# Kernel optimization log

Measured on AMD Instinct MI355X. Metric: run time of the kernel, lower is better.

Reference implementation:

```python
import jax, jax.numpy as jnp
import numpy as np

EPS = 1e-5

def _conv(x, w, b, pad):
    # x: [B,C,H,W], w: [O,I,kh,kw] -> [B,O,H',W']
    y = jax.lax.conv_general_dilated(x, w, (1, 1), pad,
                                     dimension_numbers=('NCHW', 'OIHW', 'NCHW'))
    return y + b[None, :, None, None]

def _bn(x, g, b, m, v):
    # inference-mode BatchNorm2d
    s = g / jnp.sqrt(v + EPS)
    return x * s[None, :, None, None] + (b - m * s)[None, :, None, None]

def setup_inputs():
    key = jax.random.key(0)
    ks = jax.random.split(key, 8)
    N, Cin, Cout, H, W, BS = 2, 64, 256, 512, 512, 32
    GH, GW = H // BS, W // BS
    nB = 256
    x = jax.random.normal(ks[0], (N, Cin, H, W), jnp.float32)
    rng = np.random.default_rng(0)
    flat = rng.choice(N * GH * GW, size=nB, replace=False)  # unique blocks
    idx = np.stack([flat // (GH * GW), (flat // GW) % GH, flat % GW], axis=1).astype(np.int32)
    indices = jnp.asarray(idx)             # [nB, 3] = (batch, block_row, block_col)
    mask = jnp.zeros((N, GH, GW), jnp.bool_).at[indices[:, 0], indices[:, 1], indices[:, 2]].set(True)
    def wgt(k, shape):
        return jax.random.normal(k, shape, jnp.float32) * 0.05
    z, o = jnp.zeros(Cout, jnp.float32), jnp.ones(Cout, jnp.float32)
    params = dict(
        w1=wgt(ks[1], (Cout, Cin, 1, 1)), b1=z, g1=o, be1=z, m1=z, v1=o,
        w2=wgt(ks[2], (Cout, Cout, 3, 3)), b2=z, g2=o, be2=z, m2=z, v2=o,
        w3=wgt(ks[3], (Cout, Cout, 1, 1)), b3=z, g3=o, be3=z, m3=z, v3=o,
        wd=wgt(ks[4], (Cout, Cin, 1, 1)), bd=z,
    )
    return {"x": x, "mask": mask, "indices": indices, **params,
            "block_size": 32, "block_stride": 32, "block_offset": 0}

def reference(x, mask, indices, w1, b1, g1, be1, m1, v1,
              w2, b2, g2, be2, m2, v2, w3, b3, g3, be3, m3, v3,
              wd, bd, block_size, block_stride, block_offset):
    BS = block_size
    N, Cin, H, W = x.shape
    b = indices[:, 0]
    rows = indices[:, 1, None] * block_stride + block_offset + jnp.arange(BS)  # [nB,BS]
    cols = indices[:, 2, None] * block_stride + block_offset + jnp.arange(BS)  # [nB,BS]
    ci = jnp.arange(Cin)
    # SparseGather: [nB, Cin, BS, BS]
    blocks = x[b[:, None, None, None], ci[None, :, None, None],
               rows[:, None, :, None], cols[:, None, None, :]]
    h = jax.nn.relu(_bn(_conv(blocks, w1, b1, 'VALID'), g1, be1, m1, v1))
    dense_y = jax.nn.relu(_bn(_conv(h, w2, b2, 'SAME'), g2, be2, m2, v2))
    # conv3/bn3 in the original are dead code (inplace-relu aliasing): output unused.
    ybase = _conv(x, wd, bd, 'VALID')  # downsample (in_channels != out_channels)
    Cout = ybase.shape[1]
    co = jnp.arange(Cout)
    # SparseScatter (add=False -> overwrite blocks; indices are unique)
    y = ybase.at[b[:, None, None, None], co[None, :, None, None],
                 rows[:, None, :, None], cols[:, None, None, :]].set(dense_y)
    return y
```

## Files before the change

kernel.cpp:

```cpp
#include <hip/hip_runtime.h>

#define HW 262144
#define EPSF 1e-5f

typedef __attribute__((ext_vector_type(8))) short bf16x8;
typedef __attribute__((ext_vector_type(4))) float f32x4;

__device__ __forceinline__ unsigned short f2bf(float f) {
    unsigned u = __builtin_bit_cast(unsigned, f);
    return (unsigned short)((u + 0x7FFFu + ((u >> 16) & 1u)) >> 16);
}

typedef __attribute__((address_space(3))) unsigned lds_u32_t;
typedef __attribute__((address_space(1))) const unsigned glb_u32_t;
__device__ __forceinline__ void dma16(const void* gsrc, void* ldst) {
    __builtin_amdgcn_global_load_lds((glb_u32_t*)gsrc, (lds_u32_t*)ldst, 16, 0, 0);
}

#define W2WS_OFF 0
#define W1WS_OFF 1212416
#define T1WS_OFF 1249280
#define S2WS_OFF 1250304
#define T2WS_OFF 1251328
#define WDWS_OFF 1252352
#define MSKWS_OFF 1289216

__global__ __launch_bounds__(512) void kmask(const int* __restrict__ indices,
                                             int nB, char* __restrict__ ws) {
    unsigned char* mb = (unsigned char*)(ws + MSKWS_OFF);
    const int t = threadIdx.x;
    if (t < 512) mb[t] = 0;
    __syncthreads();
    if (t < nB) {
        int bn = indices[t*3+0], gh = indices[t*3+1], gw = indices[t*3+2];
        if ((unsigned)bn < 2u && (unsigned)gh < 16u && (unsigned)gw < 16u)
            mb[bn*256 + gh*16 + gw] = 1;
    }
}

__global__ __launch_bounds__(256) void kprep(
    const float* __restrict__ w1, const float* __restrict__ b1,
    const float* __restrict__ g1, const float* __restrict__ be1,
    const float* __restrict__ m1, const float* __restrict__ v1,
    const float* __restrict__ w2, const float* __restrict__ b2,
    const float* __restrict__ g2, const float* __restrict__ be2,
    const float* __restrict__ m2, const float* __restrict__ v2,
    const float* __restrict__ wd,
    char* __restrict__ ws)
{
    unsigned short* w2ws = (unsigned short*)(ws + W2WS_OFF);
    unsigned short* w1ws = (unsigned short*)(ws + W1WS_OFF);
    unsigned short* wdws = (unsigned short*)(ws + WDWS_OFF);
    float* t1ws = (float*)(ws + T1WS_OFF);
    float* s2ws = (float*)(ws + S2WS_OFF);
    float* t2ws = (float*)(ws + T2WS_OFF);

    const int bid = blockIdx.x, t = threadIdx.x;
    if (bid < 2304) {
        int e  = bid*256 + t;
        int hc = e & 31;
        int r1 = e >> 5;
        int tap = r1 % 9;
        int r2 = r1 / 9;
        int co = r2 & 63;
        int q  = r2 >> 6;
        int cz = q & 3, ch = q >> 2;
        float v = w2[(size_t)(cz*64+co)*2304 + (size_t)(ch*32+hc)*9 + tap];
        w2ws[((ch*4+cz)*64+co)*296 + tap*32 + hc] = f2bf(v);
    } else if (bid < 2368) {
        int e = (bid-2304)*256 + t;
        int hc = e >> 6, ci = e & 63;
        float s1 = g1[hc] * rsqrtf(v1[hc] + EPSF);
        w1ws[hc*72 + ci] = f2bf(w1[hc*64+ci] * s1);
    } else if (bid < 2432) {
        int e = (bid-2368)*256 + t;
        int co = e >> 6, ci = e & 63;
        wdws[co*72 + ci] = f2bf(wd[co*64 + ci]);
    } else {
        if (t < 256) {
            float s1 = g1[t] * rsqrtf(v1[t] + EPSF);
            t1ws[t] = (b1[t]-m1[t])*s1 + be1[t];
            float s2 = g2[t] * rsqrtf(v2[t] + EPSF);
            s2ws[t] = s2;
            t2ws[t] = (b2[t]-m2[t])*s2 + be2[t];
        }
    }
}

__global__ __launch_bounds__(256, 2) void k1_mfma(
    const float* __restrict__ x,
    const float* __restrict__ bd, const char* __restrict__ ws,
    const int* __restrict__ bstride, const int* __restrict__ boff,
    float* __restrict__ y)
{
    extern __shared__ char smem[];
    unsigned short* xT  = (unsigned short*)smem;
    unsigned short* wdS = (unsigned short*)(smem + 36864);
    float*          bdS = (float*)(smem + 73728);

    const int t = threadIdx.x, lane = t & 63, w = t >> 6;
    const int m = lane & 15, g = lane >> 4;
    const int bid = blockIdx.x;
    const int n   = bid >> 10;
    const int row = (bid >> 1) & 511;
    const int c0  = (bid & 1) * 256;

    #pragma unroll
    for (int i = 0; i < 9; ++i)
        dma16((const char*)ws + WDWS_OFF + (t + i*256)*16,
              (char*)wdS + (t + i*256)*16);
    if (t < 64) dma16((const char*)bd + t*16, (char*)bdS + t*16);

    const size_t xbase = (size_t)n*64*HW + (size_t)row*512 + c0;
    #pragma unroll 4
    for (int jc = 0; jc < 16; ++jc) {
        int ci = w + 4*jc;
        float4 xv = *(const float4*)&x[xbase + (size_t)ci*HW + lane*4];
        xT[(lane*4+0)*72 + ci] = f2bf(xv.x);
        xT[(lane*4+1)*72 + ci] = f2bf(xv.y);
        xT[(lane*4+2)*72 + ci] = f2bf(xv.z);
        xT[(lane*4+3)*72 + ci] = f2bf(xv.w);
    }

    const int stride = bstride[0], off = boff[0];
    const bool safe = (stride == 32) && (off == 0);
    unsigned long long mv = 0;
    if (safe) {
        const unsigned char* mb = (const unsigned char*)(ws + MSKWS_OFF);
        mv = *(const unsigned long long*)&mb[n*256 + (row>>5)*16 + (bid&1)*8];
    }

    __syncthreads();

    bf16x8 bF[2][4];
    #pragma unroll
    for (int pxf = 0; pxf < 4; ++pxf)
        #pragma unroll
        for (int kk = 0; kk < 2; ++kk)
            bF[kk][pxf] = *(const bf16x8*)&xT[(w*64 + pxf*16 + m)*72 + kk*32 + g*8];

    const size_t ybase = (size_t)(n*256)*HW + (size_t)row*512 + c0;
    #pragma unroll 1
    for (int cof = 0; cof < 16; ++cof) {
        bf16x8 a0 = *(const bf16x8*)&wdS[(cof*16+m)*72 +      g*8];
        bf16x8 a1 = *(const bf16x8*)&wdS[(cof*16+m)*72 + 32 + g*8];
        f32x4 ac[4];
        #pragma unroll
        for (int pxf = 0; pxf < 4; ++pxf) {
            ac[pxf] = (f32x4){0.f,0.f,0.f,0.f};
            ac[pxf] = __builtin_amdgcn_mfma_f32_16x16x32_bf16(a0, bF[0][pxf], ac[pxf], 0, 0, 0);
            ac[pxf] = __builtin_amdgcn_mfma_f32_16x16x32_bf16(a1, bF[1][pxf], ac[pxf], 0, 0, 0);
        }
        #pragma unroll
        for (int pxf = 0; pxf < 4; ++pxf) {
            const int pxg = w*4 + pxf;
            const bool skip = safe && (((mv >> ((pxg>>1)*8)) & 0xffull) != 0ull);
            if (!skip) {
                #pragma unroll
                for (int j = 0; j < 4; ++j) {
                    const int co = cof*16 + g*4 + j;
                    y[ybase + (size_t)co*HW + pxg*16 + m] = ac[pxf][j] + bdS[co];
                }
            }
        }
    }
}

__global__ __launch_bounds__(512, 2) void k2_fused(
    const float* __restrict__ x, const int* __restrict__ indices,
    const char* __restrict__ ws,
    const int* __restrict__ bstride, const int* __restrict__ boff,
    float* __restrict__ y)
{
    extern __shared__ char smem[];
    unsigned short* xT  = (unsigned short*)smem;
    unsigned short* w1s = (unsigned short*)(smem + 50688);
    unsigned short* hS  = (unsigned short*)(smem + 55296);
    unsigned short* w2S = (unsigned short*)(smem + 77824);
    float* t1S = (float*)(smem + 115712);
    float* s2S = (float*)(smem + 116736);
    float* t2S = (float*)(smem + 117760);

    const unsigned short* w2ws = (const unsigned short*)(ws + W2WS_OFF);
    const unsigned short* w1ws = (const unsigned short*)(ws + W1WS_OFF);

    const int t    = threadIdx.x;
    const int lane = t & 63;
    const int w    = t >> 6;
    const int m    = lane & 15;
    const int g    = lane >> 4;

    const int bid = blockIdx.x;
    const int blk = bid >> 2, pz = bid & 3;
    const int bn = indices[blk*3+0], gr = indices[blk*3+1], gc = indices[blk*3+2];
    const int stride = bstride[0], off = boff[0];
    const int row0 = gr*stride + off, col0 = gc*stride + off;

    if (t < 192) {
        const float* src = (t < 64) ? (const float*)(ws + T1WS_OFF)
                         : (t < 128) ? (const float*)(ws + S2WS_OFF)
                                     : (const float*)(ws + T2WS_OFF);
        float* dst = (t < 64) ? t1S : (t < 128) ? s2S : t2S;
        dma16(src + (lane)*4, dst + (lane)*4);
    }

    {
        const int half = lane >> 5, cc = lane & 31;
        for (int pb = w*80; pb < w*80 + 80; pb += 2) {
            int pi = pb + half;
            int r = pi >> 6, ci = pi & 63;
            int br = pz*8 + r - 1;
            if ((unsigned)br < 32u) {
                float xv = x[(size_t)bn*64*HW + (size_t)ci*HW
                             + (size_t)(row0+br)*512 + (col0+cc)];
                xT[(r*34 + cc + 1)*72 + ci] = f2bf(xv);
            }
        }
    }

    f32x4 acc[4][2][4];
    #pragma unroll
    for (int a = 0; a < 4; ++a)
        #pragma unroll
        for (int b = 0; b < 2; ++b)
            #pragma unroll
            for (int c = 0; c < 4; ++c) acc[a][b][c] = (f32x4){0.f,0.f,0.f,0.f};

    #pragma unroll 1
    for (int ch = 0; ch < 8; ++ch) {
        __syncthreads();

        if (t < 288) dma16((const char*)w1ws + ch*4608 + t*16, (char*)w1s + t*16);
        {
            const char* ws2 = (const char*)w2ws + (size_t)(ch*4 + 0)*37888;
            #pragma unroll
            for (int i = 0; i < 4; ++i)
                dma16(ws2 + t*16 + i*8192, (char*)w2S + t*16 + i*8192);
            if (t < 320) dma16(ws2 + t*16 + 32768, (char*)w2S + t*16 + 32768);
        }
        __syncthreads();

        f32x4 a1[3][2];
        #pragma unroll
        for (int i = 0; i < 3; ++i) { a1[i][0] = (f32x4){0,0,0,0}; a1[i][1] = (f32x4){0,0,0,0}; }
        #pragma unroll
        for (int i = 0; i < 3; ++i) {
            const int tile = w*3 + i;
            if (tile < 22) {
                #pragma unroll
                for (int kk = 0; kk < 2; ++kk) {
                    bf16x8 bF = *(const bf16x8*)&xT[(tile*16 + m)*72 + kk*32 + g*8];
                    #pragma unroll
                    for (int hct = 0; hct < 2; ++hct) {
                        bf16x8 aF = *(const bf16x8*)&w1s[(hct*16 + m)*72 + kk*32 + g*8];
                        a1[i][hct] = __builtin_amdgcn_mfma_f32_16x16x32_bf16(
                                         aF, bF, a1[i][hct], 0, 0, 0);
                    }
                }
            }
        }
        #pragma unroll
        for (int i = 0; i < 3; ++i) {
            const int tile = w*3 + i;
            if (tile < 22) {
                int p = tile*16 + m;
                int r = p / 34;
                int c = p - r*34;
                int br = pz*8 + r - 1;
                bool valid = (c >= 1) && (c <= 32) && ((unsigned)br < 32u);
                #pragma unroll
                for (int hct = 0; hct < 2; ++hct) {
                    unsigned short hv[4];
                    #pragma unroll
                    for (int j = 0; j < 4; ++j) {
                        float tv = t1S[ch*32 + hct*16 + g*4 + j];
                        float hf = fmaxf(a1[i][hct][j] + tv, 0.f);
                        hv[j] = valid ? f2bf(hf) : (unsigned short)0;
                    }
                    unsigned lo = (unsigned)hv[0] | ((unsigned)hv[1] << 16);
                    unsigned hi = (unsigned)hv[2] | ((unsigned)hv[3] << 16);
                    *(uint2*)&hS[p*32 + hct*16 + g*4] = make_uint2(lo, hi);
                }
            }
        }
        __syncthreads();

        #pragma unroll
        for (int cz = 0; cz < 4; ++cz) {
            #pragma unroll
            for (int tap = 0; tap < 9; ++tap) {
                const int dy = tap/3, dx = tap%3;
                bf16x8 aF[4];
                #pragma unroll
                for (int cof = 0; cof < 4; ++cof)
                    aF[cof] = *(const bf16x8*)&w2S[(cof*16 + m)*296 + tap*32 + g*8];
                #pragma unroll
                for (int pxf = 0; pxf < 2; ++pxf) {
                    int p = (w + dy)*34 + pxf*16 + m + dx;
                    bf16x8 bF = *(const bf16x8*)&hS[p*32 + g*8];
                    if (cz == 0) {
                        #pragma unroll
                        for (int cof = 0; cof < 4; ++cof)
                            acc[0][pxf][cof] = __builtin_amdgcn_mfma_f32_16x16x32_bf16(
                                aF[cof], bF, acc[0][pxf][cof], 0, 0, 0);
                    } else if (cz == 1) {
                        #pragma unroll
                        for (int cof = 0; cof < 4; ++cof)
                            acc[1][pxf][cof] = __builtin_amdgcn_mfma_f32_16x16x32_bf16(
                                aF[cof], bF, acc[1][pxf][cof], 0, 0, 0);
                    } else if (cz == 2) {
                        #pragma unroll
                        for (int cof = 0; cof < 4; ++cof)
                            acc[2][pxf][cof] = __builtin_amdgcn_mfma_f32_16x16x32_bf16(
                                aF[cof], bF, acc[2][pxf][cof], 0, 0, 0);
                    } else {
                        #pragma unroll
                        for (int cof = 0; cof < 4; ++cof)
                            acc[3][pxf][cof] = __builtin_amdgcn_mfma_f32_16x16x32_bf16(
                                aF[cof], bF, acc[3][pxf][cof], 0, 0, 0);
                    }
                }
            }
            if (cz < 3) {
                __syncthreads();
                const char* ws2 = (const char*)w2ws + (size_t)(ch*4 + cz + 1)*37888;
                #pragma unroll
                for (int i2 = 0; i2 < 4; ++i2)
                    dma16(ws2 + t*16 + i2*8192, (char*)w2S + t*16 + i2*8192);
                if (t < 320) dma16(ws2 + t*16 + 32768, (char*)w2S + t*16 + 32768);
                __syncthreads();
            }
        }
    }

    const size_t ybase = (size_t)bn*256*HW + (size_t)(row0 + pz*8 + w)*512 + col0;
    #pragma unroll
    for (int cz = 0; cz < 4; ++cz) {
        #pragma unroll
        for (int cof = 0; cof < 4; ++cof) {
            #pragma unroll
            for (int j = 0; j < 4; ++j) {
                const int co = cz*64 + cof*16 + g*4 + j;
                float s2 = s2S[co], t2 = t2S[co];
                #pragma unroll
                for (int pxf = 0; pxf < 2; ++pxf) {
                    y[ybase + (size_t)co*HW + pxf*16 + m] =
                        fmaxf(fmaf(acc[cz][pxf][cof][j], s2, t2), 0.f);
                }
            }
        }
    }
}

extern "C" void kernel_launch(void* const* d_in, const int* in_sizes, int n_in,
                              void* d_out, int out_size, void* d_ws, size_t ws_size,
                              hipStream_t stream) {
    const float* x       = (const float*)d_in[0];
    const int*   indices = (const int*)  d_in[2];
    const float* w1  = (const float*)d_in[3];
    const float* b1  = (const float*)d_in[4];
    const float* g1  = (const float*)d_in[5];
    const float* be1 = (const float*)d_in[6];
    const float* m1  = (const float*)d_in[7];
    const float* v1  = (const float*)d_in[8];
    const float* w2  = (const float*)d_in[9];
    const float* b2  = (const float*)d_in[10];
    const float* g2  = (const float*)d_in[11];
    const float* be2 = (const float*)d_in[12];
    const float* m2  = (const float*)d_in[13];
    const float* v2  = (const float*)d_in[14];
    const float* wd  = (const float*)d_in[21];
    const float* bd  = (const float*)d_in[22];
    const int* bstride = (const int*)d_in[24];
    const int* boff    = (const int*)d_in[25];
    float* y = (float*)d_out;
    char* ws = (char*)d_ws;

    const int nB = in_sizes[2] / 3;

    hipLaunchKernelGGL(kmask, dim3(1), dim3(512), 0, stream, indices, nB, ws);
    hipLaunchKernelGGL(kprep, dim3(2433), dim3(256), 0, stream,
                       w1, b1, g1, be1, m1, v1, w2, b2, g2, be2, m2, v2, wd, ws);
    hipLaunchKernelGGL(k1_mfma, dim3(2048), dim3(256), 74752, stream,
                       x, bd, ws, bstride, boff, y);
    hipLaunchKernelGGL(k2_fused, dim3(nB * 4), dim3(512), 118784, stream,
                       x, indices, ws, bstride, boff, y);
}
```

Before: 537.3 us.

## Double-buffer conv2 weight tiles in LDS and pad the hidden-activation stride

Conv2 weight slices now go into two LDS buffers. The DMA for the next-but-one slice is issued while the current slice is being multiplied, which removes half of the barrier pairs per channel chunk and overlaps the weight loads with MFMA work. The hidden-activation row stride goes from 32 to 40 bf16 elements, meant to cut LDS bank conflicts on B-fragment reads. s_setprio is raised around the MFMA loops. The trade-off is more LDS per block (about 162 KB), close to the per-CU limit.

Measured after the change: 504.1 us. -6.2%, faster.

```diff
diff --git a/kernel.cpp b/kernel.cpp
--- a/kernel.cpp
+++ b/kernel.cpp
@@ -166,6 +166,38 @@
     }
 }
 
+#define DMA_W2(CH, CZ, BUF)                                                   \
+    {                                                                         \
+        const char* ws2_ = (const char*)w2ws + (size_t)((CH)*4 + (CZ))*37888; \
+        _Pragma("unroll")                                                     \
+        for (int i2_ = 0; i2_ < 4; ++i2_)                                     \
+            dma16(ws2_ + t*16 + i2_*8192, (char*)(BUF) + t*16 + i2_*8192);    \
+        if (t < 320) dma16(ws2_ + t*16 + 32768, (char*)(BUF) + t*16 + 32768); \
+    }
+
+#define CONV2_CZ(CZ, BUF)                                                     \
+    {                                                                         \
+        __builtin_amdgcn_s_setprio(1);                                        \
+        _Pragma("unroll")                                                     \
+        for (int tap = 0; tap < 9; ++tap) {                                   \
+            const int dy = tap/3, dx = tap%3;                                 \
+            bf16x8 aF[4];                                                     \
+            _Pragma("unroll")                                                 \
+            for (int cof = 0; cof < 4; ++cof)                                 \
+                aF[cof] = *(const bf16x8*)&(BUF)[(cof*16 + m)*296 + tap*32 + g*8]; \
+            _Pragma("unroll")                                                 \
+            for (int pxf = 0; pxf < 2; ++pxf) {                               \
+                int p_ = (w + dy)*34 + pxf*16 + m + dx;                       \
+                bf16x8 bFr = *(const bf16x8*)&hS[p_*40 + g*8];                \
+                _Pragma("unroll")                                             \
+                for (int cof = 0; cof < 4; ++cof)                             \
+                    acc[CZ][pxf][cof] = __builtin_amdgcn_mfma_f32_16x16x32_bf16( \
+                        aF[cof], bFr, acc[CZ][pxf][cof], 0, 0, 0);            \
+            }                                                                 \
+        }                                                                     \
+        __builtin_amdgcn_s_setprio(0);                                        \
+    }
+
 __global__ __launch_bounds__(512, 2) void k2_fused(
     const float* __restrict__ x, const int* __restrict__ indices,
     const char* __restrict__ ws,
@@ -176,10 +208,11 @@
     unsigned short* xT  = (unsigned short*)smem;
     unsigned short* w1s = (unsigned short*)(smem + 50688);
     unsigned short* hS  = (unsigned short*)(smem + 55296);
-    unsigned short* w2S = (unsigned short*)(smem + 77824);
-    float* t1S = (float*)(smem + 115712);
-    float* s2S = (float*)(smem + 116736);
-    float* t2S = (float*)(smem + 117760);
+    unsigned short* w2A = (unsigned short*)(smem + 83456);
+    unsigned short* w2B = (unsigned short*)(smem + 121344);
+    float* t1S = (float*)(smem + 159232);
+    float* s2S = (float*)(smem + 160256);
+    float* t2S = (float*)(smem + 161280);
 
     const unsigned short* w2ws = (const unsigned short*)(ws + W2WS_OFF);
     const unsigned short* w1ws = (const unsigned short*)(ws + W1WS_OFF);
@@ -231,13 +264,8 @@
         __syncthreads();
 
         if (t < 288) dma16((const char*)w1ws + ch*4608 + t*16, (char*)w1s + t*16);
-        {
-            const char* ws2 = (const char*)w2ws + (size_t)(ch*4 + 0)*37888;
-            #pragma unroll
-            for (int i = 0; i < 4; ++i)
-                dma16(ws2 + t*16 + i*8192, (char*)w2S + t*16 + i*8192);
-            if (t < 320) dma16(ws2 + t*16 + 32768, (char*)w2S + t*16 + 32768);
-        }
+        DMA_W2(ch, 0, w2A);
+        DMA_W2(ch, 1, w2B);
         __syncthreads();
 
         f32x4 a1[3][2];
@@ -279,58 +307,21 @@
                     }
                     unsigned lo = (unsigned)hv[0] | ((unsigned)hv[1] << 16);
                     unsigned hi = (unsigned)hv[2] | ((unsigned)hv[3] << 16);
-                    *(uint2*)&hS[p*32 + hct*16 + g*4] = make_uint2(lo, hi);
+                    *(uint2*)&hS[p*40 + hct*16 + g*4] = make_uint2(lo, hi);
                 }
             }
         }
         __syncthreads();
 
-        #pragma unroll
-        for (int cz = 0; cz < 4; ++cz) {
-            #pragma unroll
-            for (int tap = 0; tap < 9; ++tap) {
-                const int dy = tap/3, dx = tap%3;
-                bf16x8 aF[4];
-                #pragma unroll
-                for (int cof = 0; cof < 4; ++cof)
-                    aF[cof] = *(const bf16x8*)&w2S[(cof*16 + m)*296 + tap*32 + g*8];
-                #pragma unroll
-                for (int pxf = 0; pxf < 2; ++pxf) {
-                    int p = (w + dy)*34 + pxf*16 + m + dx;
-                    bf16x8 bF = *(const bf16x8*)&hS[p*32 + g*8];
-                    if (cz == 0) {
-                        #pragma unroll
-                        for (int cof = 0; cof < 4; ++cof)
-                            acc[0][pxf][cof] = __builtin_amdgcn_mfma_f32_16x16x32_bf16(
-                                aF[cof], bF, acc[0][pxf][cof], 0, 0, 0);
-                    } else if (cz == 1) {
-                        #pragma unroll
-                        for (int cof = 0; cof < 4; ++cof)
-                            acc[1][pxf][cof] = __builtin_amdgcn_mfma_f32_16x16x32_bf16(
-                                aF[cof], bF, acc[1][pxf][cof], 0, 0, 0);
-                    } else if (cz == 2) {
-                        #pragma unroll
-                        for (int cof = 0; cof < 4; ++cof)
-                            acc[2][pxf][cof] = __builtin_amdgcn_mfma_f32_16x16x32_bf16(
-                                aF[cof], bF, acc[2][pxf][cof], 0, 0, 0);
-                    } else {
-                        #pragma unroll
-                        for (int cof = 0; cof < 4; ++cof)
-                            acc[3][pxf][cof] = __builtin_amdgcn_mfma_f32_16x16x32_bf16(
-                                aF[cof], bF, acc[3][pxf][cof], 0, 0, 0);
-                    }
-                }
-            }
-            if (cz < 3) {
-                __syncthreads();
-                const char* ws2 = (const char*)w2ws + (size_t)(ch*4 + cz + 1)*37888;
-                #pragma unroll
-                for (int i2 = 0; i2 < 4; ++i2)
-                    dma16(ws2 + t*16 + i2*8192, (char*)w2S + t*16 + i2*8192);
-                if (t < 320) dma16(ws2 + t*16 + 32768, (char*)w2S + t*16 + 32768);
-                __syncthreads();
-            }
-        }
+        CONV2_CZ(0, w2A);
+        __syncthreads();
+        DMA_W2(ch, 2, w2A);
+        CONV2_CZ(1, w2B);
+        __syncthreads();
+        DMA_W2(ch, 3, w2B);
+        CONV2_CZ(2, w2A);
+        __syncthreads();
+        CONV2_CZ(3, w2B);
     }
 
     const size_t ybase = (size_t)bn*256*HW + (size_t)(row0 + pz*8 + w)*512 + col0;
@@ -383,6 +374,6 @@
                        w1, b1, g1, be1, m1, v1, w2, b2, g2, be2, m2, v2, wd, ws);
     hipLaunchKernelGGL(k1_mfma, dim3(2048), dim3(256), 74752, stream,
                        x, bd, ws, bstride, boff, y);
-    hipLaunchKernelGGL(k2_fused, dim3(nB * 4), dim3(512), 118784, stream,
+    hipLaunchKernelGGL(k2_fused, dim3(nB * 4), dim3(512), 162304, stream,
                        x, indices, ws, bstride, boff, y);
 }
```
